# Optimization experiments

Hardware: AMD Instinct MI355X
Metric: run time of the kernel (lower is better)

The kernel has to match this reference:

```python
import jax, jax.numpy as jnp
import numpy as np

N_NODES = 50000
N_EDGES = 800000
N_REL = 8
OUT_CH = 64      # latent dim of z
HID = 128        # hidden_channels
IN_CH = 128      # reconstructed feature dim
NEG_SLOPE = 0.2


def rgat_conv(x, src, dst, edge_type, weight, q, k, bias, num_nodes):
    """PyG RGATConv, heads=1, dim=1, additive-self-attention, across-relation.
    x: [N, in]; weight: [R, in, out]; q,k: [out, 1]; bias: [out]."""
    # per-relation transform of all nodes, then per-edge gather (same math as
    # per-edge bmm with weight[edge_type], avoids [E, in, out] intermediate)
    x_all = jnp.einsum('ni,rio->nro', x, weight)          # [N, R, out]
    x_j = x_all[src, edge_type]                            # [E, out]
    x_i = x_all[dst, edge_type]                            # [E, out]
    alpha = (x_i @ q + x_j @ k)[:, 0]                      # [E]
    alpha = jax.nn.leaky_relu(alpha, NEG_SLOPE)
    # scatter-softmax over destination neighborhoods
    m = jax.ops.segment_max(alpha, dst, num_segments=num_nodes)
    m = jnp.where(jnp.isfinite(m), m, 0.0)                 # empty segments -> 0
    ex = jnp.exp(alpha - m[dst])
    denom = jax.ops.segment_sum(ex, dst, num_segments=num_nodes)
    a = ex / (denom[dst] + 1e-16)                          # [E]
    out = jax.ops.segment_sum(a[:, None] * x_j, dst, num_segments=num_nodes)
    return out + bias


def setup_inputs() -> dict:
    key = jax.random.key(0)
    ks = jax.random.split(key, 12)
    z = jax.random.normal(ks[0], (N_NODES, OUT_CH), dtype=jnp.float32)
    edge_index = jax.random.randint(ks[1], (2, N_EDGES), 0, N_NODES, dtype=jnp.int32)
    edge_type = jax.random.randint(ks[2], (N_EDGES,), 0, N_REL, dtype=jnp.int32)

    def glorot(k_, shape):
        fan = shape[-2] + shape[-1]
        return jax.random.normal(k_, shape, dtype=jnp.float32) * jnp.sqrt(2.0 / fan)

    return {
        'z': z,
        'lin_w': glorot(ks[3], (HID, OUT_CH)),
        'lin_b': jnp.zeros((HID,), dtype=jnp.float32),
        'w1': glorot(ks[4], (N_REL, HID, HID)),
        'q1': glorot(ks[5], (HID, 1)),
        'k1': glorot(ks[6], (HID, 1)),
        'b1': jnp.zeros((HID,), dtype=jnp.float32),
        'w2': glorot(ks[7], (N_REL, HID, IN_CH)),
        'q2': glorot(ks[8], (IN_CH, 1)),
        'k2': glorot(ks[9], (IN_CH, 1)),
        'b2': jnp.zeros((IN_CH,), dtype=jnp.float32),
        'edge_index': edge_index,
        'edge_type': edge_type,
    }


def reference(z, lin_w, lin_b, w1, q1, k1, b1, w2, q2, k2, b2, edge_index, edge_type):
    num_nodes = z.shape[0]
    src, dst = edge_index[0], edge_index[1]
    h = z @ lin_w.T + lin_b                                 # nn.Linear
    h = jax.nn.relu(rgat_conv(h, src, dst, edge_type, w1, q1, k1, b1, num_nodes))
    # dropout is identity in eval mode
    recon_x = rgat_conv(h, src, dst, edge_type, w2, q2, k2, b2, num_nodes)
    return recon_x
```

## Files before the change

kernel.cpp:

```cpp
#include <hip/hip_runtime.h>
#include <hip/hip_bf16.h>
#include <cstdint>
#include <cstddef>

#define N_NODES 50000
#define N_EDGES 800000
#define NSEG    (N_NODES * 8)

using frag_t = __attribute__((ext_vector_type(8))) short;
using f32x4  = __attribute__((ext_vector_type(4))) float;

typedef const __attribute__((address_space(1))) void* gptr_t;
typedef __attribute__((address_space(3))) void* lptr_t;

__device__ __forceinline__ short f2bf(float x) {
    __hip_bfloat16 h = __float2bfloat16(x);
    return *reinterpret_cast<short*>(&h);
}
__device__ __forceinline__ float bf2f(unsigned int u) {
    union { unsigned int i; float f; } v;
    v.i = u << 16;
    return v.f;
}
__device__ __forceinline__ unsigned int packbf2(float lo, float hi) {
    unsigned int a = (unsigned short)f2bf(lo);
    unsigned int b = (unsigned short)f2bf(hi);
    return a | (b << 16);
}


__global__ void hist_kernel(const int* __restrict__ dst, const int* __restrict__ et,
                            int* __restrict__ deg8, int E) {
    int e = blockIdx.x * 256 + threadIdx.x;
    if (e < E) atomicAdd(&deg8[dst[e] * 8 + et[e]], 1);
}

__global__ __launch_bounds__(256) void scan_part(const int* __restrict__ deg8,
                                                 int* __restrict__ part, int M) {
    __shared__ int red[256];
    int t = threadIdx.x;
    int idx = blockIdx.x * 1024 + t * 4;
    int s = 0;
    if (idx + 3 < M) {
        int4 d = *(const int4*)(deg8 + idx);
        s = d.x + d.y + d.z + d.w;
    } else {
        for (int c = 0; c < 4; c++) if (idx + c < M) s += deg8[idx + c];
    }
    red[t] = s;
    __syncthreads();
    #pragma unroll
    for (int off = 128; off; off >>= 1) {
        if (t < off) red[t] += red[t + off];
        __syncthreads();
    }
    if (t == 0) part[blockIdx.x] = red[0];
}

__global__ __launch_bounds__(512) void scan_mid(int* __restrict__ part, int nparts,
                                                int* __restrict__ rowp, int M) {
    __shared__ int buf[512];
    int t = threadIdx.x;
    int own = (t < nparts) ? part[t] : 0;
    buf[t] = own;
    __syncthreads();
    for (int off = 1; off < 512; off <<= 1) {
        int v = buf[t];
        int u = (t >= off) ? buf[t - off] : 0;
        __syncthreads();
        buf[t] = v + u;
        __syncthreads();
    }
    if (t < nparts) part[t] = buf[t] - own;
    if (t == 511) rowp[M] = buf[511];
}

__global__ __launch_bounds__(256) void scan_fix(const int* __restrict__ deg8,
                                                const int* __restrict__ part,
                                                int* __restrict__ rowp,
                                                int* __restrict__ cursor, int M) {
    __shared__ int wsum[4];
    int t = threadIdx.x, lane = t & 63, w = t >> 6;
    int idx = blockIdx.x * 1024 + t * 4;
    int v0 = 0, v1 = 0, v2 = 0, v3 = 0;
    if (idx + 3 < M) {
        int4 d = *(const int4*)(deg8 + idx);
        v0 = d.x; v1 = d.y; v2 = d.z; v3 = d.w;
    } else {
        if (idx     < M) v0 = deg8[idx];
        if (idx + 1 < M) v1 = deg8[idx + 1];
        if (idx + 2 < M) v2 = deg8[idx + 2];
        if (idx + 3 < M) v3 = deg8[idx + 3];
    }
    int tsum = v0 + v1 + v2 + v3;
    int sc = tsum;
    #pragma unroll
    for (int off = 1; off < 64; off <<= 1) {
        int u = __shfl_up(sc, off, 64);
        if (lane >= off) sc += u;
    }
    if (lane == 63) wsum[w] = sc;
    __syncthreads();
    int woff = 0;
    for (int i = 0; i < w; i++) woff += wsum[i];
    int excl = part[blockIdx.x] + woff + sc - tsum;
    if (idx     < M) { rowp[idx]     = excl; cursor[idx]     = excl; } excl += v0;
    if (idx + 1 < M) { rowp[idx + 1] = excl; cursor[idx + 1] = excl; } excl += v1;
    if (idx + 2 < M) { rowp[idx + 2] = excl; cursor[idx + 2] = excl; } excl += v2;
    if (idx + 3 < M) { rowp[idx + 3] = excl; cursor[idx + 3] = excl; }
}

__global__ void fill_kernel(const int* __restrict__ src, const int* __restrict__ dst,
                            const int* __restrict__ et, int* __restrict__ cursor,
                            int* __restrict__ sorted, int E) {
    int e = blockIdx.x * 256 + threadIdx.x;
    if (e < E) {
        int pos = atomicAdd(&cursor[dst[e] * 8 + et[e]], 1);
        sorted[pos] = src[e] | (et[e] << 16);
    }
}


__global__ __launch_bounds__(256) void gemm_lin(const float* __restrict__ A,
                                                const float* __restrict__ B,
                                                const float* __restrict__ bias,
                                                unsigned short* __restrict__ hb, int N) {
    const int Kdim = 64;
    __shared__ float As[32][64];
    __shared__ float Bs[32][128];
    int t = threadIdx.x;
    int n0 = blockIdx.x * 64;
    int rg = t >> 4, cg = t & 15;
    int an = t >> 2, ak = (t & 3) * 8;
    float acc[4][8] = {};

    for (int k0 = 0; k0 < Kdim; k0 += 32) {
        int gn = n0 + an;
        if (gn < N) {
            const float* ap = A + (size_t)gn * Kdim + k0 + ak;
            float4 v0 = *(const float4*)ap;
            float4 v1 = *(const float4*)(ap + 4);
            As[ak + 0][an] = v0.x; As[ak + 1][an] = v0.y;
            As[ak + 2][an] = v0.z; As[ak + 3][an] = v0.w;
            As[ak + 4][an] = v1.x; As[ak + 5][an] = v1.y;
            As[ak + 6][an] = v1.z; As[ak + 7][an] = v1.w;
        } else {
            #pragma unroll
            for (int c = 0; c < 8; c++) As[ak + c][an] = 0.f;
        }
        {
            int o = t >> 1, kh = (t & 1) * 16;
            const float* bp = B + (size_t)o * Kdim + k0 + kh;
            #pragma unroll
            for (int j = 0; j < 4; j++) {
                float4 v = ((const float4*)bp)[j];
                Bs[kh + j * 4 + 0][o] = v.x;
                Bs[kh + j * 4 + 1][o] = v.y;
                Bs[kh + j * 4 + 2][o] = v.z;
                Bs[kh + j * 4 + 3][o] = v.w;
            }
        }
        __syncthreads();
        #pragma unroll
        for (int k = 0; k < 32; k++) {
            float a[4], b[8];
            *(float4*)&a[0] = *(const float4*)&As[k][rg * 4];
            *(float4*)&b[0] = *(const float4*)&Bs[k][cg * 8];
            *(float4*)&b[4] = *(const float4*)&Bs[k][cg * 8 + 4];
            #pragma unroll
            for (int i = 0; i < 4; i++)
                #pragma unroll
                for (int j = 0; j < 8; j++)
                    acc[i][j] = fmaf(a[i], b[j], acc[i][j]);
        }
        __syncthreads();
    }
    #pragma unroll
    for (int i = 0; i < 4; i++) {
        int gn = n0 + rg * 4 + i;
        if (gn < N) {
            unsigned short us[8];
            #pragma unroll
            for (int j = 0; j < 8; j++)
                us[j] = (unsigned short)f2bf(acc[i][j] + bias[cg * 8 + j]);
            *(int4*)(hb + (size_t)gn * 128 + cg * 8) = *(int4*)&us[0];
        }
    }
}


__global__ void wprep_kernel(const float* __restrict__ W, const float* __restrict__ q,
                             const float* __restrict__ k, short* __restrict__ Bf,
                             float* __restrict__ wq, float* __restrict__ wk) {
    int g = blockIdx.x * 256 + threadIdx.x;
    if (g < 131072) {
        int kk = g >> 7, o = g & 127;
        float v = W[(size_t)kk * 128 + o];
        Bf[(((size_t)(kk >> 3) * 128) + o) * 8 + (kk & 7)] = f2bf(v);
        return;
    }
    int h = g - 131072;
    if (h < 2048) {
        int which = h >> 10;
        int r = (h >> 7) & 7;
        int i = h & 127;
        const float* vec = which ? k : q;
        const float* wrow = W + ((size_t)r * 128 + i) * 128;
        float acc = 0.f;
        #pragma unroll 4
        for (int o = 0; o < 128; o++) acc = fmaf(wrow[o], vec[o], acc);
        (which ? wk : wq)[r * 128 + i] = acc;
    }
}


__global__ __launch_bounds__(256) void qk_table_kernel(const unsigned short* __restrict__ xb,
                                                       const float* __restrict__ wq,
                                                       const float* __restrict__ wk,
                                                       float* __restrict__ Q,
                                                       float* __restrict__ K, int N) {
    int n = blockIdx.x * 256 + threadIdx.x;
    if (n >= N) return;
    const uint2* row = (const uint2*)(xb + (size_t)n * 128);
    float aq[8] = {}, ak[8] = {};
    for (int i = 0; i < 32; i++) {
        uint2 d = row[i];
        float x0 = bf2f(d.x & 0xFFFFu);
        float x1 = bf2f(d.x >> 16);
        float x2 = bf2f(d.y & 0xFFFFu);
        float x3 = bf2f(d.y >> 16);
        int c = i * 4;
        #pragma unroll
        for (int r = 0; r < 8; r++) {
            const float* wqr = wq + r * 128 + c;
            const float* wkr = wk + r * 128 + c;
            aq[r] = fmaf(x0, wqr[0], fmaf(x1, wqr[1], fmaf(x2, wqr[2], fmaf(x3, wqr[3], aq[r]))));
            ak[r] = fmaf(x0, wkr[0], fmaf(x1, wkr[1], fmaf(x2, wkr[2], fmaf(x3, wkr[3], ak[r]))));
        }
    }
    float4* qp = (float4*)(Q + (size_t)n * 8);
    qp[0] = *(float4*)&aq[0];
    qp[1] = *(float4*)&aq[4];
    float4* kp = (float4*)(K + (size_t)n * 8);
    kp[0] = *(float4*)&ak[0];
    kp[1] = *(float4*)&ak[4];
}


__global__ __launch_bounds__(256) void agg_s_kernel(const unsigned short* __restrict__ hb,
                                                    const float* __restrict__ Q,
                                                    const float* __restrict__ Kt,
                                                    const int* __restrict__ rowp8,
                                                    const int* __restrict__ sorted,
                                                    short* __restrict__ s, int N) {
    int wv = threadIdx.x >> 6;
    int lane = threadIdx.x & 63;
    int n = blockIdx.x * 4 + wv;
    if (n >= N) return;
    int beg = rowp8[n * 8];
    int end = rowp8[n * 8 + 8];
    int deg = end - beg;
    unsigned int* spw = (unsigned int*)(s + (size_t)n * 1024);
    const unsigned int* hbu = (const unsigned int*)hb;

    if (deg == 0) {
        int4 z = {0, 0, 0, 0};
        int4* p = (int4*)spw;
        p[lane * 2]     = z;
        p[lane * 2 + 1] = z;
        return;
    }

    float2 acc = {0.f, 0.f};
    int rcur = 0;

    if (deg <= 64) {
        int pk = 0;
        float a = -INFINITY;
        if (lane < deg) {
            pk = sorted[beg + lane];
            int srcn = pk & 0xFFFF, etj = pk >> 16;
            a = Q[(size_t)n * 8 + etj] + Kt[(size_t)srcn * 8 + etj];
            a = (a > 0.f) ? a : 0.2f * a;
        }
        float m = a;
        #pragma unroll
        for (int off = 32; off; off >>= 1) m = fmaxf(m, __shfl_xor(m, off, 64));
        float e = (lane < deg) ? __expf(a - m) : 0.f;
        float sum = e;
        #pragma unroll
        for (int off = 32; off; off >>= 1) sum += __shfl_xor(sum, off, 64);
        float w = e / (sum + 1e-16f);

        int j = 0;
        for (; j + 8 <= deg; j += 8) {
            int pp[8]; float ww[8]; unsigned int dd[8];
            #pragma unroll
            for (int i = 0; i < 8; i++) {
                pp[i] = __shfl(pk, j + i, 64);
                ww[i] = __shfl(w,  j + i, 64);
            }
            #pragma unroll
            for (int i = 0; i < 8; i++)
                dd[i] = hbu[(size_t)(pp[i] & 0xFFFF) * 64 + lane];
            #pragma unroll
            for (int i = 0; i < 8; i++) {
                int e0 = pp[i] >> 16;
                while (rcur < e0) { spw[rcur * 64 + lane] = packbf2(acc.x, acc.y); acc.x = acc.y = 0.f; rcur++; }
                acc.x = fmaf(ww[i], bf2f(dd[i] & 0xFFFF), acc.x);
                acc.y = fmaf(ww[i], bf2f(dd[i] >> 16),    acc.y);
            }
        }
        for (; j < deg; j++) {
            int   p0 = __shfl(pk, j, 64);
            float w0 = __shfl(w, j, 64);
            unsigned int d0 = hbu[(size_t)(p0 & 0xFFFF) * 64 + lane];
            int e0 = p0 >> 16;
            while (rcur < e0) { spw[rcur * 64 + lane] = packbf2(acc.x, acc.y); acc.x = acc.y = 0.f; rcur++; }
            acc.x = fmaf(w0, bf2f(d0 & 0xFFFF), acc.x);
            acc.y = fmaf(w0, bf2f(d0 >> 16),    acc.y);
        }
        while (rcur < 8) { spw[rcur * 64 + lane] = packbf2(acc.x, acc.y); acc.x = acc.y = 0.f; rcur++; }
        return;
    }

    auto logit = [&](int j) -> float {
        int pk = sorted[beg + j];
        int srcn = pk & 0xFFFF, etj = pk >> 16;
        float a = Q[(size_t)n * 8 + etj] + Kt[(size_t)srcn * 8 + etj];
        return (a > 0.f) ? a : 0.2f * a;
    };
    float m = -INFINITY;
    for (int j = lane; j < deg; j += 64) m = fmaxf(m, logit(j));
    #pragma unroll
    for (int off = 32; off; off >>= 1) m = fmaxf(m, __shfl_xor(m, off, 64));
    float sum = 0.f;
    for (int j = lane; j < deg; j += 64) sum += __expf(logit(j) - m);
    #pragma unroll
    for (int off = 32; off; off >>= 1) sum += __shfl_xor(sum, off, 64);
    float inv = 1.f / (sum + 1e-16f);

    for (int j0 = 0; j0 < deg; j0 += 64) {
        int cnt = min(64, deg - j0);
        int pk = 0;
        float w = 0.f;
        if (lane < cnt) {
            pk = sorted[beg + j0 + lane];
            int srcn = pk & 0xFFFF, etj = pk >> 16;
            float a = Q[(size_t)n * 8 + etj] + Kt[(size_t)srcn * 8 + etj];
            a = (a > 0.f) ? a : 0.2f * a;
            w = __expf(a - m) * inv;
        }
        for (int j = 0; j < cnt; j++) {
            int   p0 = __shfl(pk, j, 64);
            float w0 = __shfl(w, j, 64);
            unsigned int d0 = hbu[(size_t)(p0 & 0xFFFF) * 64 + lane];
            int e0 = p0 >> 16;
            while (rcur < e0) { spw[rcur * 64 + lane] = packbf2(acc.x, acc.y); acc.x = acc.y = 0.f; rcur++; }
            acc.x = fmaf(w0, bf2f(d0 & 0xFFFF), acc.x);
            acc.y = fmaf(w0, bf2f(d0 >> 16),    acc.y);
        }
    }
    while (rcur < 8) { spw[rcur * 64 + lane] = packbf2(acc.x, acc.y); acc.x = acc.y = 0.f; rcur++; }
}


__global__ __launch_bounds__(256) void gemm_mfma(const short* __restrict__ s,
                                                 const short* __restrict__ Bf,
                                                 const float* __restrict__ bias,
                                                 float* __restrict__ Cout,
                                                 unsigned short* __restrict__ hbout,
                                                 int N, int relu) {
    __shared__ short As[4096];
    __shared__ short Bs[4096];
    int t = threadIdx.x;
    int w = t >> 6, lane = t & 63;
    int lhi = lane >> 4, llo = lane & 15;
    int n0 = blockIdx.x * 128;
    const char* sB = (const char*)s;
    const char* bB = (const char*)Bf;
    f32x4 acc[16] = {};

    for (int c = 0; c < 32; c++) {
        #pragma unroll
        for (int i = 0; i < 2; i++) {
            int row = i * 64 + lane;
            const void* gp = sB + (size_t)(n0 + row) * 2048 + c * 64 + w * 16;
            __builtin_amdgcn_global_load_lds(
                (gptr_t)gp, (lptr_t)((char*)As + w * 2048 + i * 1024), 16, 0, 0);
        }
        #pragma unroll
        for (int i = 0; i < 2; i++) {
            const void* gp = bB + (size_t)c * 8192 + w * 2048 + i * 1024 + lane * 16;
            __builtin_amdgcn_global_load_lds(
                (gptr_t)gp, (lptr_t)((char*)Bs + w * 2048 + i * 1024), 16, 0, 0);
        }
        __syncthreads();
        frag_t a0 = *(const frag_t*)(As + ((size_t)lhi * 128 + w * 32 + llo) * 8);
        frag_t a1 = *(const frag_t*)(As + ((size_t)lhi * 128 + w * 32 + llo + 16) * 8);
        #pragma unroll
        for (int ct = 0; ct < 8; ct++) {
            frag_t b = *(const frag_t*)(Bs + ((size_t)lhi * 128 + ct * 16 + llo) * 8);
            acc[ct]     = __builtin_amdgcn_mfma_f32_16x16x32_bf16(a0, b, acc[ct], 0, 0, 0);
            acc[8 + ct] = __builtin_amdgcn_mfma_f32_16x16x32_bf16(a1, b, acc[8 + ct], 0, 0, 0);
        }
        __syncthreads();
    }
    #pragma unroll
    for (int rt = 0; rt < 2; rt++) {
        #pragma unroll
        for (int ct = 0; ct < 8; ct++) {
            int col = ct * 16 + llo;
            float bv = bias[col];
            #pragma unroll
            for (int rg = 0; rg < 4; rg++) {
                int rown = n0 + w * 32 + rt * 16 + lhi * 4 + rg;
                if (rown < N) {
                    float v = acc[rt * 8 + ct][rg] + bv;
                    if (relu) v = fmaxf(v, 0.f);
                    if (Cout)  Cout[(size_t)rown * 128 + col] = v;
                    if (hbout) hbout[(size_t)rown * 128 + col] = (unsigned short)f2bf(v);
                }
            }
        }
    }
}


extern "C" void kernel_launch(void* const* d_in, const int* in_sizes, int n_in,
                              void* d_out, int out_size, void* d_ws, size_t ws_size,
                              hipStream_t stream) {
    const float* z     = (const float*)d_in[0];
    const float* lin_w = (const float*)d_in[1];
    const float* lin_b = (const float*)d_in[2];
    const float* w1    = (const float*)d_in[3];
    const float* q1    = (const float*)d_in[4];
    const float* k1    = (const float*)d_in[5];
    const float* b1    = (const float*)d_in[6];
    const float* w2    = (const float*)d_in[7];
    const float* q2    = (const float*)d_in[8];
    const float* k2    = (const float*)d_in[9];
    const float* b2    = (const float*)d_in[10];
    const int*   ei    = (const int*)d_in[11];
    const int*   et    = (const int*)d_in[12];
    float* out = (float*)d_out;

    char* ws = (char*)d_ws;
    size_t off = 0;
    auto alloc = [&](size_t bytes) -> void* {
        void* p = ws + off;
        off += (bytes + 255) & ~(size_t)255;
        return p;
    };
    short* s     = (short*)alloc((size_t)N_NODES * 1024 * 2);
    unsigned short* hb = (unsigned short*)alloc((size_t)N_NODES * 128 * 2);
    float* Q     = (float*)alloc((size_t)N_NODES * 8 * 4);
    float* K     = (float*)alloc((size_t)N_NODES * 8 * 4);
    int* sorted  = (int*)alloc((size_t)N_EDGES * 4);
    int* deg8    = (int*)alloc((size_t)NSEG * 4);
    int* rowp8   = (int*)alloc((size_t)(NSEG + 1) * 4);
    int* cursor8 = (int*)alloc((size_t)NSEG * 4);
    int* part    = (int*)alloc(1024 * 4);
    float* wq    = (float*)alloc(8 * 128 * 4);
    float* wk    = (float*)alloc(8 * 128 * 4);
    short* Bf    = (short*)alloc((size_t)1024 * 128 * 2);

    const int* src = ei;
    const int* dst = ei + N_EDGES;

    const int M = NSEG;
    const int nparts = (M + 1023) / 1024;

    hipMemsetAsync(deg8, 0, (size_t)M * 4, stream);
    hist_kernel<<<(N_EDGES + 255) / 256, 256, 0, stream>>>(dst, et, deg8, N_EDGES);
    scan_part<<<nparts, 256, 0, stream>>>(deg8, part, M);
    scan_mid<<<1, 512, 0, stream>>>(part, nparts, rowp8, M);
    scan_fix<<<nparts, 256, 0, stream>>>(deg8, part, rowp8, cursor8, M);
    fill_kernel<<<(N_EDGES + 255) / 256, 256, 0, stream>>>(src, dst, et, cursor8, sorted, N_EDGES);

    gemm_lin<<<(N_NODES + 63) / 64, 256, 0, stream>>>(z, lin_w, lin_b, hb, N_NODES);

    int mgrid = (N_NODES + 127) / 128;
    int agrid = (N_NODES + 3) / 4;
    int qgrid = (N_NODES + 255) / 256;
    int wgrid = (131072 + 2048) / 256;

    wprep_kernel<<<wgrid, 256, 0, stream>>>(w1, q1, k1, Bf, wq, wk);
    qk_table_kernel<<<qgrid, 256, 0, stream>>>(hb, wq, wk, Q, K, N_NODES);
    agg_s_kernel<<<agrid, 256, 0, stream>>>(hb, Q, K, rowp8, sorted, s, N_NODES);
    gemm_mfma<<<mgrid, 256, 0, stream>>>(s, Bf, b1, (float*)nullptr, hb, N_NODES, 1);

    wprep_kernel<<<wgrid, 256, 0, stream>>>(w2, q2, k2, Bf, wq, wk);
    qk_table_kernel<<<qgrid, 256, 0, stream>>>(hb, wq, wk, Q, K, N_NODES);
    agg_s_kernel<<<agrid, 256, 0, stream>>>(hb, Q, K, rowp8, sorted, s, N_NODES);
    gemm_mfma<<<mgrid, 256, 0, stream>>>(s, Bf, b2, out, (unsigned short*)nullptr, N_NODES, 0);
}
```

Measured before the change: 413.9 us.

## Fuse attention aggregation with MFMA GEMM via LDS-resident per-relation tile

The separate aggregation kernel, which wrote a 50000x1024 bf16 per-relation intermediate to global memory, is merged with the MFMA GEMM that read it back. Each 512-thread block now aggregates 32 nodes into a swizzled 64KB LDS tile and immediately multiplies it by the stacked relation weights, streaming B tiles through LDS. The aim is to remove roughly 200MB of global write and read traffic per layer plus one launch. In exchange the large LDS footprint limits occupancy, the GEMM tile per block is small, and the output needs a second hb buffer to avoid a read/write race.

```diff
diff --git a/kernel.cpp b/kernel.cpp
--- a/kernel.cpp
+++ b/kernel.cpp
@@ -247,180 +247,175 @@
 }
 
 
-__global__ __launch_bounds__(256) void agg_s_kernel(const unsigned short* __restrict__ hb,
-                                                    const float* __restrict__ Q,
-                                                    const float* __restrict__ Kt,
-                                                    const int* __restrict__ rowp8,
-                                                    const int* __restrict__ sorted,
-                                                    short* __restrict__ s, int N) {
-    int wv = threadIdx.x >> 6;
-    int lane = threadIdx.x & 63;
-    int n = blockIdx.x * 4 + wv;
-    if (n >= N) return;
-    int beg = rowp8[n * 8];
-    int end = rowp8[n * 8 + 8];
-    int deg = end - beg;
-    unsigned int* spw = (unsigned int*)(s + (size_t)n * 1024);
+__global__ __launch_bounds__(512, 4) void fused_agg_gemm(
+        const unsigned short* __restrict__ hb,
+        const float* __restrict__ Q,
+        const float* __restrict__ Kt,
+        const int* __restrict__ rowp8,
+        const int* __restrict__ sorted,
+        const short* __restrict__ Bf,
+        const float* __restrict__ bias,
+        float* __restrict__ Cout,
+        unsigned short* __restrict__ hbout,
+        int N, int relu) {
+    __shared__ short s_tile[32 * 1024];
+    __shared__ short Bsh[8192];
+    unsigned int* sdw = (unsigned int*)s_tile;
     const unsigned int* hbu = (const unsigned int*)hb;
 
-    if (deg == 0) {
-        int4 z = {0, 0, 0, 0};
-        int4* p = (int4*)spw;
-        p[lane * 2]     = z;
-        p[lane * 2 + 1] = z;
-        return;
-    }
-
-    float2 acc = {0.f, 0.f};
-    int rcur = 0;
-
-    if (deg <= 64) {
-        int pk = 0;
-        float a = -INFINITY;
-        if (lane < deg) {
-            pk = sorted[beg + lane];
-            int srcn = pk & 0xFFFF, etj = pk >> 16;
-            a = Q[(size_t)n * 8 + etj] + Kt[(size_t)srcn * 8 + etj];
-            a = (a > 0.f) ? a : 0.2f * a;
-        }
-        float m = a;
-        #pragma unroll
-        for (int off = 32; off; off >>= 1) m = fmaxf(m, __shfl_xor(m, off, 64));
-        float e = (lane < deg) ? __expf(a - m) : 0.f;
-        float sum = e;
-        #pragma unroll
-        for (int off = 32; off; off >>= 1) sum += __shfl_xor(sum, off, 64);
-        float w = e / (sum + 1e-16f);
-
-        int j = 0;
-        for (; j + 8 <= deg; j += 8) {
-            int pp[8]; float ww[8]; unsigned int dd[8];
-            #pragma unroll
-            for (int i = 0; i < 8; i++) {
-                pp[i] = __shfl(pk, j + i, 64);
-                ww[i] = __shfl(w,  j + i, 64);
-            }
-            #pragma unroll
-            for (int i = 0; i < 8; i++)
-                dd[i] = hbu[(size_t)(pp[i] & 0xFFFF) * 64 + lane];
-            #pragma unroll
-            for (int i = 0; i < 8; i++) {
-                int e0 = pp[i] >> 16;
-                while (rcur < e0) { spw[rcur * 64 + lane] = packbf2(acc.x, acc.y); acc.x = acc.y = 0.f; rcur++; }
-                acc.x = fmaf(ww[i], bf2f(dd[i] & 0xFFFF), acc.x);
-                acc.y = fmaf(ww[i], bf2f(dd[i] >> 16),    acc.y);
-            }
-        }
-        for (; j < deg; j++) {
-            int   p0 = __shfl(pk, j, 64);
-            float w0 = __shfl(w, j, 64);
-            unsigned int d0 = hbu[(size_t)(p0 & 0xFFFF) * 64 + lane];
-            int e0 = p0 >> 16;
-            while (rcur < e0) { spw[rcur * 64 + lane] = packbf2(acc.x, acc.y); acc.x = acc.y = 0.f; rcur++; }
-            acc.x = fmaf(w0, bf2f(d0 & 0xFFFF), acc.x);
-            acc.y = fmaf(w0, bf2f(d0 >> 16),    acc.y);
-        }
-        while (rcur < 8) { spw[rcur * 64 + lane] = packbf2(acc.x, acc.y); acc.x = acc.y = 0.f; rcur++; }
-        return;
-    }
-
-    auto logit = [&](int j) -> float {
-        int pk = sorted[beg + j];
-        int srcn = pk & 0xFFFF, etj = pk >> 16;
-        float a = Q[(size_t)n * 8 + etj] + Kt[(size_t)srcn * 8 + etj];
-        return (a > 0.f) ? a : 0.2f * a;
-    };
-    float m = -INFINITY;
-    for (int j = lane; j < deg; j += 64) m = fmaxf(m, logit(j));
-    #pragma unroll
-    for (int off = 32; off; off >>= 1) m = fmaxf(m, __shfl_xor(m, off, 64));
-    float sum = 0.f;
-    for (int j = lane; j < deg; j += 64) sum += __expf(logit(j) - m);
-    #pragma unroll
-    for (int off = 32; off; off >>= 1) sum += __shfl_xor(sum, off, 64);
-    float inv = 1.f / (sum + 1e-16f);
-
-    for (int j0 = 0; j0 < deg; j0 += 64) {
-        int cnt = min(64, deg - j0);
-        int pk = 0;
-        float w = 0.f;
-        if (lane < cnt) {
-            pk = sorted[beg + j0 + lane];
-            int srcn = pk & 0xFFFF, etj = pk >> 16;
-            float a = Q[(size_t)n * 8 + etj] + Kt[(size_t)srcn * 8 + etj];
-            a = (a > 0.f) ? a : 0.2f * a;
-            w = __expf(a - m) * inv;
-        }
-        for (int j = 0; j < cnt; j++) {
-            int   p0 = __shfl(pk, j, 64);
-            float w0 = __shfl(w, j, 64);
-            unsigned int d0 = hbu[(size_t)(p0 & 0xFFFF) * 64 + lane];
-            int e0 = p0 >> 16;
-            while (rcur < e0) { spw[rcur * 64 + lane] = packbf2(acc.x, acc.y); acc.x = acc.y = 0.f; rcur++; }
-            acc.x = fmaf(w0, bf2f(d0 & 0xFFFF), acc.x);
-            acc.y = fmaf(w0, bf2f(d0 >> 16),    acc.y);
-        }
-    }
-    while (rcur < 8) { spw[rcur * 64 + lane] = packbf2(acc.x, acc.y); acc.x = acc.y = 0.f; rcur++; }
-}
-
-
-__global__ __launch_bounds__(256) void gemm_mfma(const short* __restrict__ s,
-                                                 const short* __restrict__ Bf,
-                                                 const float* __restrict__ bias,
-                                                 float* __restrict__ Cout,
-                                                 unsigned short* __restrict__ hbout,
-                                                 int N, int relu) {
-    __shared__ short As[4096];
-    __shared__ short Bs[4096];
     int t = threadIdx.x;
     int w = t >> 6, lane = t & 63;
     int lhi = lane >> 4, llo = lane & 15;
-    int n0 = blockIdx.x * 128;
-    const char* sB = (const char*)s;
-    const char* bB = (const char*)Bf;
-    f32x4 acc[16] = {};
-
-    for (int c = 0; c < 32; c++) {
+    int n0 = blockIdx.x * 32;
+
+    for (int nd = 0; nd < 4; nd++) {
+        int row = w * 4 + nd;
+        int n = n0 + row;
+        float2 acc = {0.f, 0.f};
+        int rcur = 0;
+        auto flushw = [&](unsigned int val) {
+            int kb = rcur * 16 + (lane >> 2);
+            sdw[kb * 128 + ((row ^ (kb & 7)) * 4) + (lane & 3)] = val;
+        };
+        if (n >= N) {
+            while (rcur < 8) { flushw(0u); rcur++; }
+            continue;
+        }
+        int beg = rowp8[n * 8];
+        int end = rowp8[n * 8 + 8];
+        int deg = end - beg;
+        if (deg == 0) {
+            while (rcur < 8) { flushw(0u); rcur++; }
+            continue;
+        }
+
+        if (deg <= 64) {
+            int pk = 0;
+            float a = -INFINITY;
+            if (lane < deg) {
+                pk = sorted[beg + lane];
+                int srcn = pk & 0xFFFF, etj = pk >> 16;
+                a = Q[(size_t)n * 8 + etj] + Kt[(size_t)srcn * 8 + etj];
+                a = (a > 0.f) ? a : 0.2f * a;
+            }
+            float m = a;
+            #pragma unroll
+            for (int off = 32; off; off >>= 1) m = fmaxf(m, __shfl_xor(m, off, 64));
+            float e = (lane < deg) ? __expf(a - m) : 0.f;
+            float sum = e;
+            #pragma unroll
+            for (int off = 32; off; off >>= 1) sum += __shfl_xor(sum, off, 64);
+            float wgt = e / (sum + 1e-16f);
+
+            int j = 0;
+            for (; j + 8 <= deg; j += 8) {
+                int pp[8]; float ww[8]; unsigned int dd[8];
+                #pragma unroll
+                for (int i = 0; i < 8; i++) {
+                    pp[i] = __shfl(pk, j + i, 64);
+                    ww[i] = __shfl(wgt, j + i, 64);
+                }
+                #pragma unroll
+                for (int i = 0; i < 8; i++)
+                    dd[i] = hbu[(size_t)(pp[i] & 0xFFFF) * 64 + lane];
+                #pragma unroll
+                for (int i = 0; i < 8; i++) {
+                    int e0 = pp[i] >> 16;
+                    while (rcur < e0) { flushw(packbf2(acc.x, acc.y)); acc.x = acc.y = 0.f; rcur++; }
+                    acc.x = fmaf(ww[i], bf2f(dd[i] & 0xFFFF), acc.x);
+                    acc.y = fmaf(ww[i], bf2f(dd[i] >> 16),    acc.y);
+                }
+            }
+            for (; j < deg; j++) {
+                int   p0 = __shfl(pk, j, 64);
+                float w0 = __shfl(wgt, j, 64);
+                unsigned int d0 = hbu[(size_t)(p0 & 0xFFFF) * 64 + lane];
+                int e0 = p0 >> 16;
+                while (rcur < e0) { flushw(packbf2(acc.x, acc.y)); acc.x = acc.y = 0.f; rcur++; }
+                acc.x = fmaf(w0, bf2f(d0 & 0xFFFF), acc.x);
+                acc.y = fmaf(w0, bf2f(d0 >> 16),    acc.y);
+            }
+            while (rcur < 8) { flushw(packbf2(acc.x, acc.y)); acc.x = acc.y = 0.f; rcur++; }
+        } else {
+            auto logit = [&](int j) -> float {
+                int pk2 = sorted[beg + j];
+                int srcn = pk2 & 0xFFFF, etj = pk2 >> 16;
+                float aa = Q[(size_t)n * 8 + etj] + Kt[(size_t)srcn * 8 + etj];
+                return (aa > 0.f) ? aa : 0.2f * aa;
+            };
+            float m = -INFINITY;
+            for (int j = lane; j < deg; j += 64) m = fmaxf(m, logit(j));
+            #pragma unroll
+            for (int off = 32; off; off >>= 1) m = fmaxf(m, __shfl_xor(m, off, 64));
+            float sum = 0.f;
+            for (int j = lane; j < deg; j += 64) sum += __expf(logit(j) - m);
+            #pragma unroll
+            for (int off = 32; off; off >>= 1) sum += __shfl_xor(sum, off, 64);
+            float inv = 1.f / (sum + 1e-16f);
+
+            for (int j0 = 0; j0 < deg; j0 += 64) {
+                int cnt = min(64, deg - j0);
+                int pk = 0;
+                float wgt = 0.f;
+                if (lane < cnt) {
+                    pk = sorted[beg + j0 + lane];
+                    int srcn = pk & 0xFFFF, etj = pk >> 16;
+                    float aa = Q[(size_t)n * 8 + etj] + Kt[(size_t)srcn * 8 + etj];
+                    aa = (aa > 0.f) ? aa : 0.2f * aa;
+                    wgt = __expf(aa - m) * inv;
+                }
+                for (int j = 0; j < cnt; j++) {
+                    int   p0 = __shfl(pk, j, 64);
+                    float w0 = __shfl(wgt, j, 64);
+                    unsigned int d0 = hbu[(size_t)(p0 & 0xFFFF) * 64 + lane];
+                    int e0 = p0 >> 16;
+                    while (rcur < e0) { flushw(packbf2(acc.x, acc.y)); acc.x = acc.y = 0.f; rcur++; }
+                    acc.x = fmaf(w0, bf2f(d0 & 0xFFFF), acc.x);
+                    acc.y = fmaf(w0, bf2f(d0 >> 16),    acc.y);
+                }
+            }
+            while (rcur < 8) { flushw(packbf2(acc.x, acc.y)); acc.x = acc.y = 0.f; rcur++; }
+        }
+    }
+    __syncthreads();
+
+    int mt  = w >> 2;
+    int ctb = (w & 3) * 2;
+    f32x4 acc0 = {}, acc1 = {};
+    for (int kk2 = 0; kk2 < 16; kk2++) {
+        const char* gpb = (const char*)Bf + (size_t)kk2 * 16384 + w * 2048;
+        __builtin_amdgcn_global_load_lds((gptr_t)(gpb + lane * 16),
+                                         (lptr_t)((char*)Bsh + w * 2048), 16, 0, 0);
+        __builtin_amdgcn_global_load_lds((gptr_t)(gpb + 1024 + lane * 16),
+                                         (lptr_t)((char*)Bsh + w * 2048 + 1024), 16, 0, 0);
+        __syncthreads();
         #pragma unroll
-        for (int i = 0; i < 2; i++) {
-            int row = i * 64 + lane;
-            const void* gp = sB + (size_t)(n0 + row) * 2048 + c * 64 + w * 16;
-            __builtin_amdgcn_global_load_lds(
-                (gptr_t)gp, (lptr_t)((char*)As + w * 2048 + i * 1024), 16, 0, 0);
-        }
+        for (int h = 0; h < 2; h++) {
+            int kb = kk2 * 8 + h * 4 + lhi;
+            int row = mt * 16 + llo;
+            int ldA = kb * 128 + ((row ^ (kb & 7)) * 4);
+            frag_t a  = *(const frag_t*)((const short*)sdw + (size_t)ldA * 2);
+            frag_t b0 = *(const frag_t*)(Bsh + (((h * 4 + lhi) * 128) + ctb * 16 + llo) * 8);
+            frag_t b1 = *(const frag_t*)(Bsh + (((h * 4 + lhi) * 128) + (ctb + 1) * 16 + llo) * 8);
+            acc0 = __builtin_amdgcn_mfma_f32_16x16x32_bf16(a, b0, acc0, 0, 0, 0);
+            acc1 = __builtin_amdgcn_mfma_f32_16x16x32_bf16(a, b1, acc1, 0, 0, 0);
+        }
+        __syncthreads();
+    }
+
+    #pragma unroll
+    for (int i = 0; i < 2; i++) {
+        f32x4 av = i ? acc1 : acc0;
+        int col = (ctb + i) * 16 + llo;
+        float bv = bias[col];
         #pragma unroll
-        for (int i = 0; i < 2; i++) {
-            const void* gp = bB + (size_t)c * 8192 + w * 2048 + i * 1024 + lane * 16;
-            __builtin_amdgcn_global_load_lds(
-                (gptr_t)gp, (lptr_t)((char*)Bs + w * 2048 + i * 1024), 16, 0, 0);
-        }
-        __syncthreads();
-        frag_t a0 = *(const frag_t*)(As + ((size_t)lhi * 128 + w * 32 + llo) * 8);
-        frag_t a1 = *(const frag_t*)(As + ((size_t)lhi * 128 + w * 32 + llo + 16) * 8);
-        #pragma unroll
-        for (int ct = 0; ct < 8; ct++) {
-            frag_t b = *(const frag_t*)(Bs + ((size_t)lhi * 128 + ct * 16 + llo) * 8);
-            acc[ct]     = __builtin_amdgcn_mfma_f32_16x16x32_bf16(a0, b, acc[ct], 0, 0, 0);
-            acc[8 + ct] = __builtin_amdgcn_mfma_f32_16x16x32_bf16(a1, b, acc[8 + ct], 0, 0, 0);
-        }
-        __syncthreads();
-    }
-    #pragma unroll
-    for (int rt = 0; rt < 2; rt++) {
-        #pragma unroll
-        for (int ct = 0; ct < 8; ct++) {
-            int col = ct * 16 + llo;
-            float bv = bias[col];
-            #pragma unroll
-            for (int rg = 0; rg < 4; rg++) {
-                int rown = n0 + w * 32 + rt * 16 + lhi * 4 + rg;
-                if (rown < N) {
-                    float v = acc[rt * 8 + ct][rg] + bv;
-                    if (relu) v = fmaxf(v, 0.f);
-                    if (Cout)  Cout[(size_t)rown * 128 + col] = v;
-                    if (hbout) hbout[(size_t)rown * 128 + col] = (unsigned short)f2bf(v);
-                }
+        for (int rg = 0; rg < 4; rg++) {
+            int rown = n0 + mt * 16 + lhi * 4 + rg;
+            if (rown < N) {
+                float v = av[rg] + bv;
+                if (relu) v = fmaxf(v, 0.f);
+                if (Cout)  Cout[(size_t)rown * 128 + col] = v;
+                if (hbout) hbout[(size_t)rown * 128 + col] = (unsigned short)f2bf(v);
             }
         }
     }
@@ -452,8 +447,8 @@
         off += (bytes + 255) & ~(size_t)255;
         return p;
     };
-    short* s     = (short*)alloc((size_t)N_NODES * 1024 * 2);
-    unsigned short* hb = (unsigned short*)alloc((size_t)N_NODES * 128 * 2);
+    unsigned short* hb  = (unsigned short*)alloc((size_t)N_NODES * 128 * 2);
+    unsigned short* hb2 = (unsigned short*)alloc((size_t)N_NODES * 128 * 2);
     float* Q     = (float*)alloc((size_t)N_NODES * 8 * 4);
     float* K     = (float*)alloc((size_t)N_NODES * 8 * 4);
     int* sorted  = (int*)alloc((size_t)N_EDGES * 4);
@@ -480,18 +475,17 @@
 
     gemm_lin<<<(N_NODES + 63) / 64, 256, 0, stream>>>(z, lin_w, lin_b, hb, N_NODES);
 
-    int mgrid = (N_NODES + 127) / 128;
-    int agrid = (N_NODES + 3) / 4;
+    int fgrid = (N_NODES + 31) / 32;
     int qgrid = (N_NODES + 255) / 256;
     int wgrid = (131072 + 2048) / 256;
 
     wprep_kernel<<<wgrid, 256, 0, stream>>>(w1, q1, k1, Bf, wq, wk);
     qk_table_kernel<<<qgrid, 256, 0, stream>>>(hb, wq, wk, Q, K, N_NODES);
-    agg_s_kernel<<<agrid, 256, 0, stream>>>(hb, Q, K, rowp8, sorted, s, N_NODES);
-    gemm_mfma<<<mgrid, 256, 0, stream>>>(s, Bf, b1, (float*)nullptr, hb, N_NODES, 1);
+    fused_agg_gemm<<<fgrid, 512, 0, stream>>>(hb, Q, K, rowp8, sorted, Bf, b1,
+                                              (float*)nullptr, hb2, N_NODES, 1);
 
     wprep_kernel<<<wgrid, 256, 0, stream>>>(w2, q2, k2, Bf, wq, wk);
-    qk_table_kernel<<<qgrid, 256, 0, stream>>>(hb, wq, wk, Q, K, N_NODES);
-    agg_s_kernel<<<agrid, 256, 0, stream>>>(hb, Q, K, rowp8, sorted, s, N_NODES);
-    gemm_mfma<<<mgrid, 256, 0, stream>>>(s, Bf, b2, out, (unsigned short*)nullptr, N_NODES, 0);
-}
+    qk_table_kernel<<<qgrid, 256, 0, stream>>>(hb2, wq, wk, Q, K, N_NODES);
+    fused_agg_gemm<<<fgrid, 512, 0, stream>>>(hb2, Q, K, rowp8, sorted, Bf, b2,
+                                              out, (unsigned short*)nullptr, N_NODES, 0);
+}
```

Result: slower. 460.5 us (+11.3%).
